# Kernel tuning notes

Measured on AMD Instinct MI355X. Metric: run time of the kernel, lower is better.

## Reference

```python
import jax, jax.numpy as jnp
import numpy as np

EPS = 1e-05


def setup_inputs() -> dict:
    key = jax.random.key(0)
    k1, k2 = jax.random.split(key)
    B, H, N, D = 4, 16, 4096, 128
    x = jax.random.normal(k1, (B, H, N, D), dtype=jnp.float32)
    # learned raw (non-skew) parameter; skew-symmetrized in reference
    S_raw = jax.random.normal(k2, (H, D, D), dtype=jnp.float32) * 0.05
    return {"x": x, "S_raw": S_raw}


def reference(x, S_raw):
    # x: (B, H, N, D); S_raw: (H, D, D)
    B, H, N, D = x.shape
    S = S_raw - jnp.swapaxes(S_raw, -1, -2)          # skew-symmetric (H, D, D)
    I = jnp.eye(D, dtype=x.dtype)
    A = (1.0 + EPS) * I + S                           # I + S + eps*I
    Bmat = I - S
    # rhs: (H, D, B*N) matching torch permute/reshape/transpose
    rhs = x.transpose(1, 3, 0, 2).reshape(H, D, B * N)
    y0 = jnp.linalg.solve(A, rhs)                     # batched solve over H
    y = Bmat @ y0                                     # (H, D, B*N)
    y = y.reshape(H, D, B, N).transpose(2, 0, 3, 1)   # (B, H, N, D)
    return y
```

## Files before the change

kernel.cpp:

```cpp
#include <hip/hip_runtime.h>
#include <stdint.h>

typedef __attribute__((ext_vector_type(4))) float floatx4;
typedef __attribute__((ext_vector_type(8))) short shortx8;
typedef __attribute__((ext_vector_type(2))) __bf16 bf16x2;

#define EPSF 1e-5f

#if defined(__has_builtin)
#if __has_builtin(__builtin_amdgcn_cvt_pk_bf16_f32)
#define HAVE_CVT_PK_BF16 1
#endif
#if __has_builtin(__builtin_amdgcn_rcpf)
#define HAVE_RCPF 1
#endif
#endif

__device__ __forceinline__ unsigned int pack2_bf16(float a, float b) {
#ifdef HAVE_CVT_PK_BF16
    bf16x2 r = __builtin_amdgcn_cvt_pk_bf16_f32(a, b);
    union { bf16x2 v; unsigned int u; } cv; cv.v = r; return cv.u;
#else
    unsigned int ua = __float_as_uint(a), ub = __float_as_uint(b);
    ua = (ua + 0x7fffu + ((ua >> 16) & 1u)) >> 16;
    ub = (ub + 0x7fffu + ((ub >> 16) & 1u)) & 0xffff0000u;
    return ub | ua;
#endif
}

__device__ __forceinline__ float fast_rcp(float x) {
#ifdef HAVE_RCPF
    return __builtin_amdgcn_rcpf(x);
#else
    return 1.0f / x;
#endif
}

__global__ __launch_bounds__(512) void cayley_invert(
    const float* __restrict__ S_raw, unsigned short* __restrict__ Mb)
{
    const int h  = blockIdx.x;
    const int t  = threadIdx.x;
    const int i  = t >> 2;
    const int s  = t & 3;
    const int j0 = s << 5;
    const float* Sr = S_raw + (size_t)h * 16384;

    float loc[32];
#pragma unroll
    for (int m = 0; m < 32; ++m) {
        const int j = j0 + m;
        float v = Sr[i * 128 + j] - Sr[j * 128 + i];
        if (j == i) v += 1.0f + EPSF;
        loc[m] = v;
    }

    __shared__ __align__(16) float rowbuf[2][128];
    __shared__ float dumbuf[2][128];

    if (i == 0) {
#pragma unroll
        for (int q = 0; q < 8; ++q) {
            floatx4 w;
            w[0] = loc[q*4+0]; w[1] = loc[q*4+1]; w[2] = loc[q*4+2]; w[3] = loc[q*4+3];
            if (q == 0 && s == 0) w[0] += 1.0f;
            *(floatx4*)(&rowbuf[0][j0 + q*4]) = w;
        }
    }
    if (s == 0) {
        float dv = loc[0];
        if (i == 0) dv -= 1.0f;
        dumbuf[0][i] = dv;
    }
    __syncthreads();

    for (int kb = 0; kb < 4; ++kb) {
#pragma unroll
        for (int kk = 0; kk < 32; ++kk) {
            const int cur = kk & 1;
            const int nxt = cur ^ 1;
            const int k   = (kb << 5) + kk;

            const float wk  = rowbuf[cur][k];
            const float dum = dumbuf[cur][i];
            const float akk = wk - 1.0f;
            const float de  = dum * fast_rcp(akk);

            floatx4 rv[8];
#pragma unroll
            for (int q = 0; q < 8; ++q)
                rv[q] = *(const floatx4*)(&rowbuf[cur][j0 + q*4]);

#pragma unroll
            for (int m = 0; m < 32; ++m)
                loc[m] = fmaf(-de, rv[m >> 2][m & 3], loc[m]);

            const int kn = k + 1;
            if (kn < 128) {
                const int sp   = (kk == 31) ? kb + 1 : kb;
                const int mloc = (kk == 31) ? 0 : kk + 1;
                const int qm   = mloc >> 2, em = mloc & 3;

                if (i == kn) {
#pragma unroll
                    for (int q = 0; q < 8; ++q) {
                        floatx4 w;
                        w[0] = loc[q*4+0]; w[1] = loc[q*4+1];
                        w[2] = loc[q*4+2]; w[3] = loc[q*4+3];
                        if (q == qm && s == sp) w[em] += 1.0f;
                        *(floatx4*)(&rowbuf[nxt][j0 + q*4]) = w;
                    }
                }
                if (s == sp) {
                    float dv = loc[mloc];
                    if (i == kn) dv -= 1.0f;
                    dumbuf[nxt][i] = dv;
                }
            }
            __syncthreads();
        }
    }

    unsigned short* dst = Mb + (size_t)h * 16384 + i * 128 + j0;
#pragma unroll
    for (int q = 0; q < 4; ++q) {
        union { shortx8 v; unsigned int u[4]; } cv;
#pragma unroll
        for (int p = 0; p < 4; ++p) {
            const int m = q*8 + p*2;
            const float v0 = (2.0f + EPSF) * loc[m]   - ((j0 + m   == i) ? 1.0f : 0.0f);
            const float v1 = (2.0f + EPSF) * loc[m+1] - ((j0 + m+1 == i) ? 1.0f : 0.0f);
            cv.u[p] = pack2_bf16(v0, v1);
        }
        *(shortx8*)(dst + q*8) = cv.v;
    }
}

__global__ __launch_bounds__(256) void cayley_apply(
    const float* __restrict__ x, const unsigned short* __restrict__ Mb,
    float* __restrict__ y)
{
    const int bid  = blockIdx.x;
    const int bh   = bid >> 3;
    const int g    = bid & 7;
    const int h    = bh & 15;
    const int tid  = threadIdx.x;
    const int w    = tid >> 6;
    const int lane = tid & 63;
    const int l15  = lane & 15;
    const int quad = lane >> 4;

    __shared__ __align__(16) unsigned short Msh[128 * 136];
    __shared__ __align__(16) float obuf[4 * 16 * 68];

    {
        const unsigned short* Mg = Mb + (size_t)h * 16384;
#pragma unroll
        for (int it = 0; it < 8; ++it) {
            const int c   = tid + it * 256;
            const int row = c >> 4;
            const int cc  = (c & 15) * 8;
            *(shortx8*)(&Msh[row * 136 + cc]) = *(const shortx8*)(Mg + row * 128 + cc);
        }
    }
    __syncthreads();

    const size_t base = (size_t)bh * (4096 * 128);
    const int row0    = g * 512 + w * 128;
    const float* xw   = x + base + (size_t)(row0 + l15) * 128;
    float* ob         = obuf + w * (16 * 68);

    floatx4 xa[2][8];
#pragma unroll
    for (int ks = 0; ks < 4; ++ks) {
        xa[0][ks*2+0] = *(const floatx4*)(xw + ks*32 + quad*8);
        xa[0][ks*2+1] = *(const floatx4*)(xw + ks*32 + quad*8 + 4);
    }

#pragma unroll
    for (int t = 0; t < 8; ++t) {
        const int cur = t & 1, nxt = cur ^ 1;
        if (t < 7) {
            const float* xn = xw + (size_t)(t + 1) * (16 * 128);
#pragma unroll
            for (int ks = 0; ks < 4; ++ks) {
                xa[nxt][ks*2+0] = *(const floatx4*)(xn + ks*32 + quad*8);
                xa[nxt][ks*2+1] = *(const floatx4*)(xn + ks*32 + quad*8 + 4);
            }
        }

        shortx8 xf[4];
#pragma unroll
        for (int ks = 0; ks < 4; ++ks) {
            const floatx4 a = xa[cur][ks*2+0];
            const floatx4 b = xa[cur][ks*2+1];
            union { shortx8 v; unsigned int u[4]; } cv;
            cv.u[0] = pack2_bf16(a[0], a[1]);
            cv.u[1] = pack2_bf16(a[2], a[3]);
            cv.u[2] = pack2_bf16(b[0], b[1]);
            cv.u[3] = pack2_bf16(b[2], b[3]);
            xf[ks] = cv.v;
        }

        floatx4 acc[8];
#pragma unroll
        for (int ct = 0; ct < 8; ++ct) acc[ct] = (floatx4)0.0f;

#pragma unroll
        for (int ks = 0; ks < 4; ++ks) {
            const int ko = ks * 32 + quad * 8;
#pragma unroll
            for (int ct = 0; ct < 8; ++ct) {
                const shortx8 mf = *(const shortx8*)(&Msh[(ct*16 + l15) * 136 + ko]);
                acc[ct] = __builtin_amdgcn_mfma_f32_16x16x32_bf16(mf, xf[ks], acc[ct], 0, 0, 0);
            }
        }

        float* yt = y + base + (size_t)(row0 + t * 16) * 128;
#pragma unroll
        for (int dh = 0; dh < 2; ++dh) {
#pragma unroll
            for (int c = 0; c < 4; ++c)
                *(floatx4*)(&ob[l15 * 68 + c * 16 + quad * 4]) = acc[dh*4 + c];
#pragma unroll
            for (int j = 0; j < 4; ++j) {
                const int f   = j * 256 + lane * 4;
                const int r   = f >> 6;
                const int col = f & 63;
                const floatx4 v = *(const floatx4*)(&ob[r * 68 + col]);
                __builtin_nontemporal_store(v, (floatx4*)(yt + (size_t)r * 128 + dh * 64 + col));
            }
        }
    }
}

extern "C" void kernel_launch(void* const* d_in, const int* in_sizes, int n_in,
                              void* d_out, int out_size, void* d_ws, size_t ws_size,
                              hipStream_t stream) {
    const float* x     = (const float*)d_in[0];
    const float* S_raw = (const float*)d_in[1];
    float* y = (float*)d_out;
    unsigned short* Mb = (unsigned short*)d_ws;

    cayley_invert<<<16, 512, 0, stream>>>(S_raw, Mb);
    cayley_apply<<<64 * 8, 256, 0, stream>>>(x, Mb, y);
}
```

Baseline: 314.2 us.

## Split apply kernel into more blocks, fragment-ordered M in LDS, direct stores

The apply kernel now launches four times as many blocks, each wave handling 32 rows instead of 128. The x double-buffer prefetch is dropped, and occupancy is hinted via launch_bounds. M is stored in LDS pre-swizzled in MFMA fragment order, so each lane reads a contiguous 16-byte chunk. The LDS staging buffer for output is removed and accumulator tiles are stored straight to global memory with nontemporal stores. This trades coalesced 64-float row writes for narrower 16-byte scattered writes, and adds per-block reloads of M.

```diff
diff --git a/kernel.cpp b/kernel.cpp
--- a/kernel.cpp
+++ b/kernel.cpp
@@ -136,13 +136,13 @@
     }
 }
 
-__global__ __launch_bounds__(256) void cayley_apply(
+__global__ __launch_bounds__(256, 4) void cayley_apply(
     const float* __restrict__ x, const unsigned short* __restrict__ Mb,
     float* __restrict__ y)
 {
     const int bid  = blockIdx.x;
-    const int bh   = bid >> 3;
-    const int g    = bid & 7;
+    const int bh   = bid >> 5;
+    const int g    = bid & 31;
     const int h    = bh & 15;
     const int tid  = threadIdx.x;
     const int w    = tid >> 6;
@@ -150,50 +150,43 @@
     const int l15  = lane & 15;
     const int quad = lane >> 4;
 
-    __shared__ __align__(16) unsigned short Msh[128 * 136];
-    __shared__ __align__(16) float obuf[4 * 16 * 68];
+    __shared__ __align__(16) unsigned short Msh[2048 * 8];
 
     {
         const unsigned short* Mg = Mb + (size_t)h * 16384;
 #pragma unroll
         for (int it = 0; it < 8; ++it) {
-            const int c   = tid + it * 256;
-            const int row = c >> 4;
-            const int cc  = (c & 15) * 8;
-            *(shortx8*)(&Msh[row * 136 + cc]) = *(const shortx8*)(Mg + row * 128 + cc);
+            const int c  = tid + it * 256;
+            const int ct = c >> 8;
+            const int ks = (c >> 6) & 3;
+            const int qd = (c >> 4) & 3;
+            const int r  = (ct << 4) | (c & 15);
+            const int gq = (ks << 2) | qd;
+            *(shortx8*)(&Msh[c * 8]) = *(const shortx8*)(Mg + r * 128 + gq * 8);
         }
     }
     __syncthreads();
 
     const size_t base = (size_t)bh * (4096 * 128);
-    const int row0    = g * 512 + w * 128;
-    const float* xw   = x + base + (size_t)(row0 + l15) * 128;
-    float* ob         = obuf + w * (16 * 68);
-
-    floatx4 xa[2][8];
-#pragma unroll
-    for (int ks = 0; ks < 4; ++ks) {
-        xa[0][ks*2+0] = *(const floatx4*)(xw + ks*32 + quad*8);
-        xa[0][ks*2+1] = *(const floatx4*)(xw + ks*32 + quad*8 + 4);
-    }
-
-#pragma unroll
-    for (int t = 0; t < 8; ++t) {
-        const int cur = t & 1, nxt = cur ^ 1;
-        if (t < 7) {
-            const float* xn = xw + (size_t)(t + 1) * (16 * 128);
-#pragma unroll
-            for (int ks = 0; ks < 4; ++ks) {
-                xa[nxt][ks*2+0] = *(const floatx4*)(xn + ks*32 + quad*8);
-                xa[nxt][ks*2+1] = *(const floatx4*)(xn + ks*32 + quad*8 + 4);
-            }
+    const int row0    = g * 128 + w * 32;
+    const float* xw   = x + base + (size_t)(row0 + l15) * 128 + quad * 8;
+
+#pragma unroll
+    for (int t = 0; t < 2; ++t) {
+        const float* xt = xw + t * (16 * 128);
+
+        floatx4 xa[8];
+#pragma unroll
+        for (int ks = 0; ks < 4; ++ks) {
+            xa[ks*2+0] = *(const floatx4*)(xt + ks*32);
+            xa[ks*2+1] = *(const floatx4*)(xt + ks*32 + 4);
         }
 
         shortx8 xf[4];
 #pragma unroll
         for (int ks = 0; ks < 4; ++ks) {
-            const floatx4 a = xa[cur][ks*2+0];
-            const floatx4 b = xa[cur][ks*2+1];
+            const floatx4 a = xa[ks*2+0];
+            const floatx4 b = xa[ks*2+1];
             union { shortx8 v; unsigned int u[4]; } cv;
             cv.u[0] = pack2_bf16(a[0], a[1]);
             cv.u[1] = pack2_bf16(a[2], a[3]);
@@ -208,29 +201,17 @@
 
 #pragma unroll
         for (int ks = 0; ks < 4; ++ks) {
-            const int ko = ks * 32 + quad * 8;
 #pragma unroll
             for (int ct = 0; ct < 8; ++ct) {
-                const shortx8 mf = *(const shortx8*)(&Msh[(ct*16 + l15) * 136 + ko]);
+                const shortx8 mf = *(const shortx8*)(&Msh[((((ct << 2) | ks) << 6) | lane) * 8]);
                 acc[ct] = __builtin_amdgcn_mfma_f32_16x16x32_bf16(mf, xf[ks], acc[ct], 0, 0, 0);
             }
         }
 
-        float* yt = y + base + (size_t)(row0 + t * 16) * 128;
-#pragma unroll
-        for (int dh = 0; dh < 2; ++dh) {
-#pragma unroll
-            for (int c = 0; c < 4; ++c)
-                *(floatx4*)(&ob[l15 * 68 + c * 16 + quad * 4]) = acc[dh*4 + c];
-#pragma unroll
-            for (int j = 0; j < 4; ++j) {
-                const int f   = j * 256 + lane * 4;
-                const int r   = f >> 6;
-                const int col = f & 63;
-                const floatx4 v = *(const floatx4*)(&ob[r * 68 + col]);
-                __builtin_nontemporal_store(v, (floatx4*)(yt + (size_t)r * 128 + dh * 64 + col));
-            }
-        }
+        float* yt = y + base + (size_t)(row0 + t*16 + l15) * 128 + quad * 4;
+#pragma unroll
+        for (int ct = 0; ct < 8; ++ct)
+            __builtin_nontemporal_store(acc[ct], (floatx4*)(yt + ct*16));
     }
 }
 
@@ -243,5 +224,5 @@
     unsigned short* Mb = (unsigned short*)d_ws;
 
     cayley_invert<<<16, 512, 0, stream>>>(S_raw, Mb);
-    cayley_apply<<<64 * 8, 256, 0, stream>>>(x, Mb, y);
-}
+    cayley_apply<<<64 * 32, 256, 0, stream>>>(x, Mb, y);
+}
```

Result: no change. 319.3 us (+1.6%).
